# Optimization experiments

Hardware: AMD Instinct MI355X
Metric: run time of the kernel (lower is better)

Reference implementation:

```python
import jax, jax.numpy as jnp
import numpy as np

B, S, D, H = 2, 2048, 1024, 16
HD = D // H  # head depth


def setup_inputs() -> dict:
    key = jax.random.key(0)
    ks = jax.random.split(key, 8)
    scale = 0.02
    K = jax.random.normal(ks[0], (B, S, D), jnp.float32)
    V = jax.random.normal(ks[1], (B, S, D), jnp.float32)
    Q = jax.random.normal(ks[2], (B, S, D), jnp.float32)
    # causal additive mask: 1.0 where attention is disallowed (strict upper triangle)
    mask = jnp.broadcast_to(
        jnp.triu(jnp.ones((S, S), jnp.float32), k=1)[None, None, :, :], (B, 1, S, S)
    )
    Wk = jax.random.normal(ks[3], (D, D), jnp.float32) * scale
    Wv = jax.random.normal(ks[4], (D, D), jnp.float32) * scale
    Wq = jax.random.normal(ks[5], (D, D), jnp.float32) * scale
    Wo = jax.random.normal(ks[6], (D, D), jnp.float32) * scale
    z = jnp.zeros((D,), jnp.float32)
    return {"K": K, "V": V, "Q": Q, "mask": mask,
            "Wk": Wk, "bk": z, "Wv": Wv, "bv": z,
            "Wq": Wq, "bq": z, "Wo": Wo, "bo": z}


def _split_heads(x):  # [B,S,D] -> [B,H,S,HD]
    return x.reshape(B, S, H, HD).transpose(0, 2, 1, 3)


def reference(K, V, Q, mask, Wk, bk, Wv, bv, Wq, bq, Wo, bo):
    k = _split_heads(K @ Wk + bk)
    v = _split_heads(V @ Wv + bv)
    q = _split_heads(Q @ Wq + bq)
    # NOTE: source scales by sqrt(d_model), not sqrt(head_depth)
    logits = jnp.einsum("bhqd,bhkd->bhqk", q, k) / jnp.sqrt(jnp.float32(D))
    logits = logits + mask * (-1e9)
    attn = jax.nn.softmax(logits, axis=-1)
    out = jnp.einsum("bhqk,bhkd->bhqd", attn, v)  # [B,H,S,HD]
    out = out.transpose(0, 2, 1, 3).reshape(B, S, D)
    return out @ Wo + bo
```

## Files before the change

### kernel.cpp

```cpp
#include <hip/hip_runtime.h>
#include <hip/hip_bf16.h>

typedef unsigned short u16;
typedef unsigned int u32;
typedef unsigned long long u64;
typedef __attribute__((ext_vector_type(8))) __bf16 bf16x8;
typedef __attribute__((ext_vector_type(4))) float f32x4;

#define SEQ 2048
#define DM 1024
#define NH 16
#define HDim 64

__device__ __forceinline__ float bf_lo(u32 u) { return __uint_as_float(u << 16); }
__device__ __forceinline__ float bf_hi(u32 u) { return __uint_as_float(u & 0xffff0000u); }
__device__ __forceinline__ u16 f2bf(float f) {
    u32 u = __float_as_uint(f);
    u32 r = (u + 0x7fffu + ((u >> 16) & 1u)) >> 16;
    return (u16)r;
}
__device__ __forceinline__ float bf2f(u16 h) { return __uint_as_float(((u32)h) << 16); }

#define GLD16(g, l)                                                         \
    __builtin_amdgcn_global_load_lds(                                       \
        (const __attribute__((address_space(1))) void*)(g),                 \
        (__attribute__((address_space(3))) void*)(l), 16, 0, 0)

__device__ __forceinline__ bool detect_f32(const u32* q)
{
    const u32 w = q[threadIdx.x & 63];
    const int e0 = ((w & 0xffffu) >> 7) & 0xff;
    const int e1 = (w >> 23) & 0xff;
    const unsigned long long b = __ballot(e0 >= 0x90 || e1 >= 0x90);
    return b != 0ull;
}

__global__ __launch_bounds__(256)
void prep_all(const void* __restrict__ Qin, const void* __restrict__ Kin,
              const void* __restrict__ Vin,
              const void* __restrict__ w0, const void* __restrict__ w1,
              const void* __restrict__ w2, const void* __restrict__ w3,
              const void* __restrict__ b0, const void* __restrict__ b1,
              const void* __restrict__ b2, const void* __restrict__ b3,
              u16* __restrict__ Xall, u16* __restrict__ Wtall,
              u16* __restrict__ ball)
{
    __shared__ u16 T[64 * 66];
    const bool f = detect_f32((const u32*)Qin);
    const int t = threadIdx.x;
    const int bid = blockIdx.x;

    if (bid < 6144) {
        const int z = bid >> 11;
        const int bx = bid & 2047;
        const void* src = (z == 0) ? Qin : (z == 1) ? Kin : Vin;
        const size_t i0 = ((size_t)bx * 256 + t) * 8;
        u16* d = Xall + (size_t)z * 4194304 + i0;
        if (f) {
            const uint4* s = reinterpret_cast<const uint4*>((const float*)src + i0);
            uint4 a = s[0], b = s[1];
            u16 o[8];
            o[0] = f2bf(__uint_as_float(a.x)); o[1] = f2bf(__uint_as_float(a.y));
            o[2] = f2bf(__uint_as_float(a.z)); o[3] = f2bf(__uint_as_float(a.w));
            o[4] = f2bf(__uint_as_float(b.x)); o[5] = f2bf(__uint_as_float(b.y));
            o[6] = f2bf(__uint_as_float(b.z)); o[7] = f2bf(__uint_as_float(b.w));
            *reinterpret_cast<uint4*>(d) = *reinterpret_cast<const uint4*>(o);
        } else {
            *reinterpret_cast<uint4*>(d) =
                *reinterpret_cast<const uint4*>((const u16*)src + i0);
        }
    } else if (bid < 7168) {
        const int r = bid - 6144;
        const int z = r >> 8;
        const void* src = (z == 0) ? w0 : (z == 1) ? w1 : (z == 2) ? w2 : w3;
        const int n0 = ((r >> 4) & 15) * 64;
        const int k0 = (r & 15) * 64;
        const int c = t & 63, g = t >> 6;
        if (f) {
            const float* W = (const float*)src;
#pragma unroll
            for (int i = 0; i < 16; i++) {
                const int kl = g * 16 + i;
                T[kl * 66 + c] = f2bf(W[(size_t)(k0 + kl) * DM + n0 + c]);
            }
        } else {
            const u16* W = (const u16*)src;
#pragma unroll
            for (int i = 0; i < 16; i++) {
                const int kl = g * 16 + i;
                T[kl * 66 + c] = W[(size_t)(k0 + kl) * DM + n0 + c];
            }
        }
        __syncthreads();
        u16* dst = Wtall + (size_t)z * 1048576;
#pragma unroll
        for (int i = 0; i < 16; i++) {
            const int nl = g * 16 + i;
            dst[(size_t)(n0 + nl) * DM + k0 + c] = T[c * 66 + nl];
        }
    } else {
#pragma unroll
        for (int j = 0; j < 16; j++) {
            const int idx = t * 16 + j;
            const int z = idx >> 10, e = idx & 1023;
            const void* src = (z == 0) ? b0 : (z == 1) ? b1 : (z == 2) ? b2 : b3;
            ball[idx] = f ? f2bf(((const float*)src)[e]) : ((const u16*)src)[e];
        }
    }
}

__global__ __launch_bounds__(256)
void gemm128(const u16* __restrict__ Xall, const u16* __restrict__ Wtall,
             const u16* __restrict__ ball, u16* __restrict__ Yall,
             void* __restrict__ dout, int zbase, const u32* __restrict__ qdet)
{
    __shared__ __align__(16) u16 As[128 * 32];
    __shared__ __align__(16) u16 Bs[128 * 32];

    const int zz = zbase + blockIdx.z;
    const bool swp = (zz == 0) || (zz == 1);
    const u16* X  = Xall + ((zz == 3) ? 0 : (size_t)zz * 4194304);
    const u16* Wt = Wtall + (size_t)zz * 1048576;

    const int t    = threadIdx.x;
    const int w    = t >> 6;
    const int lane = t & 63;
    const int quad = lane >> 4;
    const int ln   = lane & 15;
    const int m0   = blockIdx.y * 128;
    const int n0   = blockIdx.x * 128;

    f32x4 acc[4][4];
#pragma unroll
    for (int i = 0; i < 4; i++)
#pragma unroll
        for (int j = 0; j < 4; j++) acc[i][j] = (f32x4){0.f, 0.f, 0.f, 0.f};

    const u16* ag = X  + (size_t)(m0 + w * 32 + (lane >> 2)) * DM + (lane & 3) * 8;
    const u16* bg = Wt + (size_t)(n0 + w * 32 + (lane >> 2)) * DM + (lane & 3) * 8;
    u16* al = &As[w * 1024];
    u16* bl = &Bs[w * 1024];

    const int wr = (w >> 1) * 64;
    const int wc = (w & 1) * 64;

    for (int kk = 0; kk < DM; kk += 32) {
        GLD16(ag,           al);
        GLD16(ag + 16 * DM, al + 512);
        GLD16(bg,           bl);
        GLD16(bg + 16 * DM, bl + 512);
        ag += 32; bg += 32;
        __syncthreads();

        bf16x8 af[4], bfr[4];
#pragma unroll
        for (int rt = 0; rt < 4; rt++)
            af[rt] = *reinterpret_cast<const bf16x8*>(&As[(wr + rt * 16 + ln) * 32 + quad * 8]);
#pragma unroll
        for (int ct = 0; ct < 4; ct++)
            bfr[ct] = *reinterpret_cast<const bf16x8*>(&Bs[(wc + ct * 16 + ln) * 32 + quad * 8]);
        if (swp) {
#pragma unroll
            for (int rt = 0; rt < 4; rt++)
#pragma unroll
                for (int ct = 0; ct < 4; ct++)
                    acc[rt][ct] = __builtin_amdgcn_mfma_f32_16x16x32_bf16(
                        bfr[ct], af[rt], acc[rt][ct], 0, 0, 0);
        } else {
#pragma unroll
            for (int rt = 0; rt < 4; rt++)
#pragma unroll
                for (int ct = 0; ct < 4; ct++)
                    acc[rt][ct] = __builtin_amdgcn_mfma_f32_16x16x32_bf16(
                        af[rt], bfr[ct], acc[rt][ct], 0, 0, 0);
        }
        __syncthreads();
    }

    u16* Y = Yall + (size_t)zz * 4194304;

    if (swp) {
        const float scale = (zz == 0) ? 0.03125f : 1.0f;
#pragma unroll
        for (int ct = 0; ct < 4; ct++) {
            const int nb = n0 + wc + ct * 16 + quad * 4;
            const int h = nb >> 6, hd = nb & (HDim - 1);
            float bv[4];
#pragma unroll
            for (int r = 0; r < 4; r++) bv[r] = bf2f(ball[zz * 1024 + nb + r]);
#pragma unroll
            for (int rt = 0; rt < 4; rt++) {
                const int m = m0 + wr + rt * 16 + ln;
                const int b = m >> 11, s = m & (SEQ - 1);
                u16 o4[4];
#pragma unroll
                for (int r = 0; r < 4; r++)
                    o4[r] = f2bf((acc[rt][ct][r] + bv[r]) * scale);
                *reinterpret_cast<u64*>(
                    Y + (((size_t)(b * NH + h)) * SEQ + s) * HDim + hd) =
                    *reinterpret_cast<const u64*>(o4);
            }
        }
    } else if (zz == 2) {
#pragma unroll
        for (int ct = 0; ct < 4; ct++) {
            const int n = n0 + wc + ct * 16 + ln;
            const float bv = bf2f(ball[zz * 1024 + n]);
            const int h = n >> 6, hd = n & (HDim - 1);
#pragma unroll
            for (int rt = 0; rt < 4; rt++) {
                const int m = m0 + wr + rt * 16 + quad * 4;
                const int b = m >> 11, s = m & (SEQ - 1);
                u16 o4[4];
#pragma unroll
                for (int r = 0; r < 4; r++) o4[r] = f2bf(acc[rt][ct][r] + bv);
                *reinterpret_cast<u64*>(
                    Y + (((size_t)(b * NH + h) * HDim + hd) * SEQ + s)) =
                    *reinterpret_cast<const u64*>(o4);
            }
        }
    } else {
        const bool f = detect_f32(qdet);
#pragma unroll
        for (int ct = 0; ct < 4; ct++) {
            const int n = n0 + wc + ct * 16 + ln;
            const float bv = bf2f(ball[zz * 1024 + n]);
#pragma unroll
            for (int rt = 0; rt < 4; rt++) {
                const int m = m0 + wr + rt * 16 + quad * 4;
#pragma unroll
                for (int r = 0; r < 4; r++) {
                    const float val = acc[rt][ct][r] + bv;
                    if (f) ((float*)dout)[(size_t)(m + r) * DM + n] = val;
                    else   ((u16*)dout)[(size_t)(m + r) * DM + n] = f2bf(val);
                }
            }
        }
    }
}

struct AttnAcc { f32x4 o[4]; float l[4]; };

__device__ __forceinline__ void attn_tile(
    const u16* __restrict__ Ks, const u16* __restrict__ Vs,
    u16* __restrict__ Ps, const bf16x8& qf0, const bf16x8& qf1,
    int kt, int rowb, int w, int quad, int ln, AttnAcc& a)
{
    f32x4 s[4];
#pragma unroll
    for (int ct = 0; ct < 4; ct++) {
        const u16* kr = &Ks[(ct * 16 + ln) * 72 + quad * 8];
        bf16x8 kf0 = *reinterpret_cast<const bf16x8*>(kr);
        bf16x8 kf1 = *reinterpret_cast<const bf16x8*>(kr + 32);
        f32x4 z = (f32x4){0.f, 0.f, 0.f, 0.f};
        z = __builtin_amdgcn_mfma_f32_16x16x32_bf16(qf0, kf0, z, 0, 0, 0);
        s[ct] = __builtin_amdgcn_mfma_f32_16x16x32_bf16(qf1, kf1, z, 0, 0, 0);
    }
#pragma unroll
    for (int ct = 0; ct < 4; ct++) {
        const int kcol = kt * 64 + ct * 16 + ln;
#pragma unroll
        for (int r = 0; r < 4; r++) {
            const float e = (kcol <= rowb + r) ? __expf(s[ct][r]) : 0.f;
            a.l[r] += e;
            Ps[(w * 16 + quad * 4 + r) * 68 + ct * 16 + ln] = f2bf(e);
        }
    }
#pragma unroll
    for (int ks = 0; ks < 2; ks++) {
        bf16x8 pf = *reinterpret_cast<const bf16x8*>(
            &Ps[(w * 16 + ln) * 68 + ks * 32 + quad * 8]);
#pragma unroll
        for (int nt = 0; nt < 4; nt++) {
            bf16x8 vf = *reinterpret_cast<const bf16x8*>(
                &Vs[(nt * 16 + ln) * 72 + ks * 32 + quad * 8]);
            a.o[nt] = __builtin_amdgcn_mfma_f32_16x16x32_bf16(pf, vf, a.o[nt], 0, 0, 0);
        }
    }
}

__global__ __launch_bounds__(256)
void attn_mfma(const u16* __restrict__ qh, const u16* __restrict__ kh,
               const u16* __restrict__ vt, u16* __restrict__ ctx)
{
    __shared__ __align__(16) u16 Ks[64 * 72];
    __shared__ __align__(16) u16 Vs[64 * 72];
    __shared__ __align__(16) u16 Ps[64 * 68];

    const int t    = threadIdx.x;
    const int i    = blockIdx.x;
    const int bh   = blockIdx.y;
    const int w    = t >> 6;
    const int lane = t & 63;
    const int quad = lane >> 4;
    const int ln   = lane & 15;
    const int qtH  = 31 - i;
    const int qtL  = i;

    const size_t kbase = (size_t)bh * SEQ * HDim;
    const size_t vbase = (size_t)bh * HDim * SEQ;

    const u16* qrH = qh + kbase + (size_t)(qtH * 64 + w * 16 + ln) * HDim;
    const bf16x8 qfH0 = *reinterpret_cast<const bf16x8*>(qrH + quad * 8);
    const bf16x8 qfH1 = *reinterpret_cast<const bf16x8*>(qrH + 32 + quad * 8);
    const u16* qrL = qh + kbase + (size_t)(qtL * 64 + w * 16 + ln) * HDim;
    const bf16x8 qfL0 = *reinterpret_cast<const bf16x8*>(qrL + quad * 8);
    const bf16x8 qfL1 = *reinterpret_cast<const bf16x8*>(qrL + 32 + quad * 8);

    AttnAcc aH, aL;
#pragma unroll
    for (int k = 0; k < 4; k++) {
        aH.o[k] = (f32x4){0.f, 0.f, 0.f, 0.f}; aH.l[k] = 0.f;
        aL.o[k] = (f32x4){0.f, 0.f, 0.f, 0.f}; aL.l[k] = 0.f;
    }

    const int srow = t >> 2;
    const int sc   = (t & 3) * 16;
    const int rowHb = qtH * 64 + w * 16 + quad * 4;
    const int rowLb = qtL * 64 + w * 16 + quad * 4;

    for (int kt = 0; kt <= qtH; kt++) {
        {
            const uint4* ks = reinterpret_cast<const uint4*>(
                kh + kbase + (size_t)(kt * 64 + srow) * HDim + sc);
            uint4* kd = reinterpret_cast<uint4*>(&Ks[srow * 72 + sc]);
            kd[0] = ks[0];
            kd[1] = ks[1];
            const uint4* vs = reinterpret_cast<const uint4*>(
                vt + vbase + (size_t)srow * SEQ + kt * 64 + sc);
            uint4* vd = reinterpret_cast<uint4*>(&Vs[srow * 72 + sc]);
            vd[0] = vs[0];
            vd[1] = vs[1];
        }
        __syncthreads();

        attn_tile(Ks, Vs, Ps, qfH0, qfH1, kt, rowHb, w, quad, ln, aH);
        if (kt <= qtL)
            attn_tile(Ks, Vs, Ps, qfL0, qfL1, kt, rowLb, w, quad, ln, aL);

        __syncthreads();
    }

#pragma unroll
    for (int m = 1; m < 16; m <<= 1) {
#pragma unroll
        for (int r = 0; r < 4; r++) {
            aH.l[r] += __shfl_xor(aH.l[r], m);
            aL.l[r] += __shfl_xor(aL.l[r], m);
        }
    }

    const int b = bh >> 4;
    const int h = bh & 15;
#pragma unroll
    for (int r = 0; r < 4; r++) {
        const float invH = 1.f / aH.l[r];
        const float invL = 1.f / aL.l[r];
        const int sH = qtH * 64 + w * 16 + quad * 4 + r;
        const int sL = qtL * 64 + w * 16 + quad * 4 + r;
        u16* dH = ctx + ((size_t)(b * SEQ + sH)) * DM + h * HDim + ln;
        u16* dL = ctx + ((size_t)(b * SEQ + sL)) * DM + h * HDim + ln;
#pragma unroll
        for (int nt = 0; nt < 4; nt++) {
            dH[nt * 16] = f2bf(aH.o[nt][r] * invH);
            dL[nt * 16] = f2bf(aL.o[nt][r] * invL);
        }
    }
}

__global__ __launch_bounds__(64)
void detect_dtype(const u32* __restrict__ q, int* __restrict__ flag)
{
    const int t = threadIdx.x;
    const u32 w = q[t];
    const int e0 = ((w & 0xffffu) >> 7) & 0xff;
    const int e1 = (w >> 23) & 0xff;
    const unsigned long long b = __ballot(e0 >= 0x90 || e1 >= 0x90);
    if (t == 0) *flag = (b != 0ull) ? 1 : 0;
}

__global__ __launch_bounds__(256)
void gemm_bias(const void* __restrict__ Xv, const void* __restrict__ Wv,
               const void* __restrict__ biasv, void* __restrict__ Yv,
               int M, int N, int K, int mode, int xsel, int wsel, int ysel,
               float scale, const int* __restrict__ flagp)
{
    __shared__ __align__(16) u16 As[64 * 32];
    __shared__ __align__(16) u16 Bs[64 * 40];

    const int f  = *flagp;
    const bool xf = (xsel != 0) && (f != 0);
    const bool wf = (wsel != 0) && (f != 0);
    const bool yf = (ysel != 0) && (f != 0);

    const u16*   Xb = (const u16*)Xv;
    const float* Xf = (const float*)Xv;
    const u16*   Wb = (const u16*)Wv;
    const float* Wf = (const float*)Wv;

    const int t    = threadIdx.x;
    const int m0   = blockIdx.y * 64;
    const int n0   = blockIdx.x * 64;
    const int w    = t >> 6;
    const int lane = t & 63;
    const int quad = lane >> 4;
    const int ln   = lane & 15;

    f32x4 acc[4];
#pragma unroll
    for (int i = 0; i < 4; i++) acc[i] = (f32x4){0.f, 0.f, 0.f, 0.f};

    const int a_row = t >> 2;
    const int a_c8  = (t & 3) * 8;
    const int b_n   = t & 63;
    const int b_k8  = (t >> 6) * 8;

    for (int kk = 0; kk < K; kk += 32) {
        const size_t aoff = (size_t)(m0 + a_row) * K + kk + a_c8;
        if (!xf) {
            *reinterpret_cast<uint4*>(&As[a_row * 32 + a_c8]) =
                *reinterpret_cast<const uint4*>(Xb + aoff);
        } else {
            const float* src = Xf + aoff;
            uint4 u0 = reinterpret_cast<const uint4*>(src)[0];
            uint4 u1 = reinterpret_cast<const uint4*>(src)[1];
            u16 tmp[8];
            tmp[0] = f2bf(__uint_as_float(u0.x));
            tmp[1] = f2bf(__uint_as_float(u0.y));
            tmp[2] = f2bf(__uint_as_float(u0.z));
            tmp[3] = f2bf(__uint_as_float(u0.w));
            tmp[4] = f2bf(__uint_as_float(u1.x));
            tmp[5] = f2bf(__uint_as_float(u1.y));
            tmp[6] = f2bf(__uint_as_float(u1.z));
            tmp[7] = f2bf(__uint_as_float(u1.w));
            *reinterpret_cast<uint4*>(&As[a_row * 32 + a_c8]) =
                *reinterpret_cast<const uint4*>(tmp);
        }
        u16 tmp[8];
        if (!wf) {
#pragma unroll
            for (int j = 0; j < 8; j++)
                tmp[j] = Wb[(size_t)(kk + b_k8 + j) * N + n0 + b_n];
        } else {
#pragma unroll
            for (int j = 0; j < 8; j++)
                tmp[j] = f2bf(Wf[(size_t)(kk + b_k8 + j) * N + n0 + b_n]);
        }
        *reinterpret_cast<uint4*>(&Bs[b_n * 40 + b_k8]) =
            *reinterpret_cast<const uint4*>(tmp);

        __syncthreads();

        bf16x8 bfrag = *reinterpret_cast<const bf16x8*>(&Bs[(w * 16 + ln) * 40 + quad * 8]);
#pragma unroll
        for (int rt = 0; rt < 4; rt++) {
            bf16x8 afrag = *reinterpret_cast<const bf16x8*>(&As[(rt * 16 + ln) * 32 + quad * 8]);
            acc[rt] = __builtin_amdgcn_mfma_f32_16x16x32_bf16(afrag, bfrag, acc[rt], 0, 0, 0);
        }
        __syncthreads();
    }

    const int n = n0 + w * 16 + ln;
    const float bv = wf ? ((const float*)biasv)[n] : bf2f(((const u16*)biasv)[n]);
#pragma unroll
    for (int rt = 0; rt < 4; rt++) {
        if (mode == 2) {
            const int m = m0 + rt * 16 + quad * 4;
            const int b = m >> 11;
            const int s = m & (SEQ - 1);
            const int h = n >> 6;
            const int hd = n & (HDim - 1);
            u16 o4[4];
#pragma unroll
            for (int r = 0; r < 4; r++) o4[r] = f2bf((acc[rt][r] + bv) * scale);
            *reinterpret_cast<u64*>(
                (u16*)Yv + (((size_t)(b * NH + h) * HDim + hd) * SEQ + s)) =
                *reinterpret_cast<const u64*>(o4);
        } else {
#pragma unroll
            for (int r = 0; r < 4; r++) {
                const int m = m0 + rt * 16 + quad * 4 + r;
                const float val = (acc[rt][r] + bv) * scale;
                if (mode == 0) {
                    if (yf) ((float*)Yv)[(size_t)m * N + n] = val;
                    else    ((u16*)Yv)[(size_t)m * N + n] = f2bf(val);
                } else {
                    const int b = m >> 11;
                    const int s = m & (SEQ - 1);
                    const int h = n >> 6;
                    const int hd = n & (HDim - 1);
                    ((u16*)Yv)[(((size_t)(b * NH + h)) * SEQ + s) * HDim + hd] = f2bf(val);
                }
            }
        }
    }
}

extern "C" void kernel_launch(void* const* d_in, const int* in_sizes, int n_in,
                              void* d_out, int out_size, void* d_ws, size_t ws_size,
                              hipStream_t stream)
{
    const void* Kin = d_in[0];
    const void* Vin = d_in[1];
    const void* Qin = d_in[2];
    const void* Wk = d_in[4];
    const void* bk = d_in[5];
    const void* Wv = d_in[6];
    const void* bv = d_in[7];
    const void* Wq = d_in[8];
    const void* bq = d_in[9];
    const void* Wo = d_in[10];
    const void* bo = d_in[11];

    char* ws = (char*)d_ws;
    const size_t NEED = ((size_t)29360128 + 4096) * 2 + 256;

    if (ws_size >= NEED) {
        u16* Xall  = (u16*)ws;
        u16* Yall  = (u16*)ws + 12582912;
        u16* Wtall = (u16*)ws + 25165824;
        u16* ball  = (u16*)ws + 29360128;
        u16* qhp   = Yall;
        u16* khp   = Yall + 4194304;
        u16* vtp   = Yall + 8388608;
        u16* ctx   = Xall;

        hipLaunchKernelGGL(prep_all, dim3(7169), dim3(256), 0, stream,
                           Qin, Kin, Vin, Wq, Wk, Wv, Wo, bq, bk, bv, bo,
                           Xall, Wtall, ball);

        hipLaunchKernelGGL(gemm128, dim3(8, 32, 3), dim3(256), 0, stream,
                           Xall, Wtall, ball, Yall, (void*)0, 0, (const u32*)Qin);

        hipLaunchKernelGGL(attn_mfma, dim3(16, 2 * NH), dim3(256), 0,
                           stream, qhp, khp, vtp, ctx);

        hipLaunchKernelGGL(gemm128, dim3(8, 32, 1), dim3(256), 0, stream,
                           Xall, Wtall, ball, Yall, d_out, 3, (const u32*)Qin);
    } else {
        const size_t SEG = (size_t)2 * SEQ * DM * sizeof(u16);
        u16* qh  = (u16*)(ws);
        u16* khd = (u16*)(ws + SEG);
        u16* vtd = (u16*)(ws + 2 * SEG);
        u16* ctx = (u16*)(ws + 3 * SEG);
        int* flag = (int*)(ws + 4 * SEG);

        hipLaunchKernelGGL(detect_dtype, dim3(1), dim3(64), 0, stream,
                           (const u32*)Qin, flag);

        const int M = 2 * SEQ;
        dim3 ggrid(DM / 64, M / 64);
        dim3 gblk(256);

        hipLaunchKernelGGL(gemm_bias, ggrid, gblk, 0, stream, Qin, Wq, bq, qh,  M, DM, DM, 1, 1, 1, 0, 0.03125f, flag);
        hipLaunchKernelGGL(gemm_bias, ggrid, gblk, 0, stream, Kin, Wk, bk, khd, M, DM, DM, 1, 1, 1, 0, 1.0f,     flag);
        hipLaunchKernelGGL(gemm_bias, ggrid, gblk, 0, stream, Vin, Wv, bv, vtd, M, DM, DM, 2, 1, 1, 0, 1.0f,     flag);

        hipLaunchKernelGGL(attn_mfma, dim3(16, 2 * NH), dim3(256), 0,
                           stream, qh, khd, vtd, ctx);

        hipLaunchKernelGGL(gemm_bias, ggrid, gblk, 0, stream, ctx, Wo, bo, d_out, M, DM, DM, 0, 0, 1, 1, 1.0f, flag);
    }
}
```

Baseline: 281.0 us.

## Fuse pipeline into cooperative persistent megakernel with split-K attention and output GEMM

Replaces the four separate launches with one cooperative persistent kernel that runs prep, QKV projection, attention, merge, output projection and reduction as phases separated by grid-wide syncs. Attention is split along the key dimension into two chunks whose unnormalized partial outputs and row sums are merged afterwards, balancing the causal workload. The output GEMM is split along K into two fp32 partial buffers that are summed with the bias. This targets launch gaps and tail imbalance, at the cost of grid-sync overhead, extra partial-result memory traffic and extra bf16 rounding of partial outputs, with a multi-kernel fallback path.

```diff
diff --git a/kernel.cpp b/kernel.cpp
--- a/kernel.cpp
+++ b/kernel.cpp
@@ -1,5 +1,8 @@
 #include <hip/hip_runtime.h>
 #include <hip/hip_bf16.h>
+#include <hip/hip_cooperative_groups.h>
+
+namespace cg = cooperative_groups;
 
 typedef unsigned short u16;
 typedef unsigned int u32;
@@ -35,21 +38,14 @@
     return b != 0ull;
 }
 
-__global__ __launch_bounds__(256)
-void prep_all(const void* __restrict__ Qin, const void* __restrict__ Kin,
-              const void* __restrict__ Vin,
-              const void* __restrict__ w0, const void* __restrict__ w1,
-              const void* __restrict__ w2, const void* __restrict__ w3,
-              const void* __restrict__ b0, const void* __restrict__ b1,
-              const void* __restrict__ b2, const void* __restrict__ b3,
-              u16* __restrict__ Xall, u16* __restrict__ Wtall,
-              u16* __restrict__ ball)
-{
-    __shared__ u16 T[64 * 66];
-    const bool f = detect_f32((const u32*)Qin);
-    const int t = threadIdx.x;
-    const int bid = blockIdx.x;
-
+
+__device__ __forceinline__ void prep_unit(
+    int bid, bool f, int t,
+    const void* Qin, const void* Kin, const void* Vin,
+    const void* w0, const void* w1, const void* w2, const void* w3,
+    const void* b0, const void* b1, const void* b2, const void* b3,
+    u16* Xall, u16* Wtall, u16* ball, u16* T)
+{
     if (bid < 6144) {
         const int z = bid >> 11;
         const int bx = bid & 2047;
@@ -107,28 +103,18 @@
             ball[idx] = f ? f2bf(((const float*)src)[e]) : ((const u16*)src)[e];
         }
     }
-}
-
-__global__ __launch_bounds__(256)
-void gemm128(const u16* __restrict__ Xall, const u16* __restrict__ Wtall,
-             const u16* __restrict__ ball, u16* __restrict__ Yall,
-             void* __restrict__ dout, int zbase, const u32* __restrict__ qdet)
-{
-    __shared__ __align__(16) u16 As[128 * 32];
-    __shared__ __align__(16) u16 Bs[128 * 32];
-
-    const int zz = zbase + blockIdx.z;
-    const bool swp = (zz == 0) || (zz == 1);
-    const u16* X  = Xall + ((zz == 3) ? 0 : (size_t)zz * 4194304);
-    const u16* Wt = Wtall + (size_t)zz * 1048576;
-
-    const int t    = threadIdx.x;
-    const int w    = t >> 6;
-    const int lane = t & 63;
-    const int quad = lane >> 4;
-    const int ln   = lane & 15;
-    const int m0   = blockIdx.y * 128;
-    const int n0   = blockIdx.x * 128;
+    __syncthreads();
+}
+
+__device__ __forceinline__ void proj_unit(
+    int zz, int m0, int n0, const u16* __restrict__ X,
+    const u16* __restrict__ Wt, const u16* __restrict__ bseg,
+    u16* __restrict__ Y, u16* SM, int t)
+{
+    u16* As = SM;
+    u16* Bs = SM + 4096;
+    const bool swp = (zz != 2);
+    const int w = t >> 6, lane = t & 63, quad = lane >> 4, ln = lane & 15;
 
     f32x4 acc[4][4];
 #pragma unroll
@@ -138,9 +124,8 @@
 
     const u16* ag = X  + (size_t)(m0 + w * 32 + (lane >> 2)) * DM + (lane & 3) * 8;
     const u16* bg = Wt + (size_t)(n0 + w * 32 + (lane >> 2)) * DM + (lane & 3) * 8;
-    u16* al = &As[w * 1024];
-    u16* bl = &Bs[w * 1024];
-
+    u16* al = As + w * 1024;
+    u16* bl = Bs + w * 1024;
     const int wr = (w >> 1) * 64;
     const int wc = (w & 1) * 64;
 
@@ -177,8 +162,6 @@
         __syncthreads();
     }
 
-    u16* Y = Yall + (size_t)zz * 4194304;
-
     if (swp) {
         const float scale = (zz == 0) ? 0.03125f : 1.0f;
 #pragma unroll
@@ -187,7 +170,7 @@
             const int h = nb >> 6, hd = nb & (HDim - 1);
             float bv[4];
 #pragma unroll
-            for (int r = 0; r < 4; r++) bv[r] = bf2f(ball[zz * 1024 + nb + r]);
+            for (int r = 0; r < 4; r++) bv[r] = bf2f(bseg[nb + r]);
 #pragma unroll
             for (int rt = 0; rt < 4; rt++) {
                 const int m = m0 + wr + rt * 16 + ln;
@@ -201,11 +184,11 @@
                     *reinterpret_cast<const u64*>(o4);
             }
         }
-    } else if (zz == 2) {
+    } else {
 #pragma unroll
         for (int ct = 0; ct < 4; ct++) {
             const int n = n0 + wc + ct * 16 + ln;
-            const float bv = bf2f(ball[zz * 1024 + n]);
+            const float bv = bf2f(bseg[n]);
             const int h = n >> 6, hd = n & (HDim - 1);
 #pragma unroll
             for (int rt = 0; rt < 4; rt++) {
@@ -219,32 +202,13 @@
                     *reinterpret_cast<const u64*>(o4);
             }
         }
-    } else {
-        const bool f = detect_f32(qdet);
-#pragma unroll
-        for (int ct = 0; ct < 4; ct++) {
-            const int n = n0 + wc + ct * 16 + ln;
-            const float bv = bf2f(ball[zz * 1024 + n]);
-#pragma unroll
-            for (int rt = 0; rt < 4; rt++) {
-                const int m = m0 + wr + rt * 16 + quad * 4;
-#pragma unroll
-                for (int r = 0; r < 4; r++) {
-                    const float val = acc[rt][ct][r] + bv;
-                    if (f) ((float*)dout)[(size_t)(m + r) * DM + n] = val;
-                    else   ((u16*)dout)[(size_t)(m + r) * DM + n] = f2bf(val);
-                }
-            }
-        }
-    }
-}
-
-struct AttnAcc { f32x4 o[4]; float l[4]; };
-
-__device__ __forceinline__ void attn_tile(
+    }
+}
+
+__device__ __forceinline__ void attn_tile2(
     const u16* __restrict__ Ks, const u16* __restrict__ Vs,
     u16* __restrict__ Ps, const bf16x8& qf0, const bf16x8& qf1,
-    int kt, int rowb, int w, int quad, int ln, AttnAcc& a)
+    int kt, int qrow, int w, int quad, int ln, f32x4* o, float& l)
 {
     f32x4 s[4];
 #pragma unroll
@@ -253,49 +217,54 @@
         bf16x8 kf0 = *reinterpret_cast<const bf16x8*>(kr);
         bf16x8 kf1 = *reinterpret_cast<const bf16x8*>(kr + 32);
         f32x4 z = (f32x4){0.f, 0.f, 0.f, 0.f};
-        z = __builtin_amdgcn_mfma_f32_16x16x32_bf16(qf0, kf0, z, 0, 0, 0);
-        s[ct] = __builtin_amdgcn_mfma_f32_16x16x32_bf16(qf1, kf1, z, 0, 0, 0);
+        z = __builtin_amdgcn_mfma_f32_16x16x32_bf16(kf0, qf0, z, 0, 0, 0);
+        s[ct] = __builtin_amdgcn_mfma_f32_16x16x32_bf16(kf1, qf1, z, 0, 0, 0);
     }
 #pragma unroll
     for (int ct = 0; ct < 4; ct++) {
-        const int kcol = kt * 64 + ct * 16 + ln;
+        u16 o4[4];
 #pragma unroll
         for (int r = 0; r < 4; r++) {
-            const float e = (kcol <= rowb + r) ? __expf(s[ct][r]) : 0.f;
-            a.l[r] += e;
-            Ps[(w * 16 + quad * 4 + r) * 68 + ct * 16 + ln] = f2bf(e);
-        }
+            const int kcol = kt * 64 + ct * 16 + quad * 4 + r;
+            const float e = (kcol <= qrow) ? __expf(s[ct][r]) : 0.f;
+            l += e;
+            o4[r] = f2bf(e);
+        }
+        *reinterpret_cast<u64*>(&Ps[(w * 16 + ln) * 72 + ct * 16 + quad * 4]) =
+            *reinterpret_cast<const u64*>(o4);
     }
 #pragma unroll
     for (int ks = 0; ks < 2; ks++) {
         bf16x8 pf = *reinterpret_cast<const bf16x8*>(
-            &Ps[(w * 16 + ln) * 68 + ks * 32 + quad * 8]);
+            &Ps[(w * 16 + ln) * 72 + ks * 32 + quad * 8]);
 #pragma unroll
         for (int nt = 0; nt < 4; nt++) {
             bf16x8 vf = *reinterpret_cast<const bf16x8*>(
                 &Vs[(nt * 16 + ln) * 72 + ks * 32 + quad * 8]);
-            a.o[nt] = __builtin_amdgcn_mfma_f32_16x16x32_bf16(pf, vf, a.o[nt], 0, 0, 0);
-        }
-    }
-}
-
-__global__ __launch_bounds__(256)
-void attn_mfma(const u16* __restrict__ qh, const u16* __restrict__ kh,
-               const u16* __restrict__ vt, u16* __restrict__ ctx)
-{
-    __shared__ __align__(16) u16 Ks[64 * 72];
-    __shared__ __align__(16) u16 Vs[64 * 72];
-    __shared__ __align__(16) u16 Ps[64 * 68];
-
-    const int t    = threadIdx.x;
-    const int i    = blockIdx.x;
-    const int bh   = blockIdx.y;
+            o[nt] = __builtin_amdgcn_mfma_f32_16x16x32_bf16(pf, vf, o[nt], 0, 0, 0);
+        }
+    }
+}
+
+__device__ __forceinline__ void attn_unit(
+    int i, int bh, int c,
+    const u16* __restrict__ qh, const u16* __restrict__ kh,
+    const u16* __restrict__ vt, u16* __restrict__ Opart,
+    float* __restrict__ Lpart, u16* SM, int t)
+{
+    u16* Ks = SM;
+    u16* Vs = SM + 4608;
+    u16* Ps = SM + 9216;
+
     const int w    = t >> 6;
     const int lane = t & 63;
     const int quad = lane >> 4;
     const int ln   = lane & 15;
     const int qtH  = 31 - i;
     const int qtL  = i;
+    const int m    = (i >= 8) ? 8 : 16 - i;
+    const int kt0  = c ? m : 0;
+    const int kt1  = c ? (qtH + 1) : m;
 
     const size_t kbase = (size_t)bh * SEQ * HDim;
     const size_t vbase = (size_t)bh * HDim * SEQ;
@@ -307,19 +276,20 @@
     const bf16x8 qfL0 = *reinterpret_cast<const bf16x8*>(qrL + quad * 8);
     const bf16x8 qfL1 = *reinterpret_cast<const bf16x8*>(qrL + 32 + quad * 8);
 
-    AttnAcc aH, aL;
+    f32x4 oH[4], oL[4];
+    float lH = 0.f, lL = 0.f;
 #pragma unroll
     for (int k = 0; k < 4; k++) {
-        aH.o[k] = (f32x4){0.f, 0.f, 0.f, 0.f}; aH.l[k] = 0.f;
-        aL.o[k] = (f32x4){0.f, 0.f, 0.f, 0.f}; aL.l[k] = 0.f;
+        oH[k] = (f32x4){0.f, 0.f, 0.f, 0.f};
+        oL[k] = (f32x4){0.f, 0.f, 0.f, 0.f};
     }
 
     const int srow = t >> 2;
     const int sc   = (t & 3) * 16;
-    const int rowHb = qtH * 64 + w * 16 + quad * 4;
-    const int rowLb = qtL * 64 + w * 16 + quad * 4;
-
-    for (int kt = 0; kt <= qtH; kt++) {
+    const int rowH = qtH * 64 + w * 16 + ln;
+    const int rowL = qtL * 64 + w * 16 + ln;
+
+    for (int kt = kt0; kt < kt1; kt++) {
         {
             const uint4* ks = reinterpret_cast<const uint4*>(
                 kh + kbase + (size_t)(kt * 64 + srow) * HDim + sc);
@@ -334,166 +304,263 @@
         }
         __syncthreads();
 
-        attn_tile(Ks, Vs, Ps, qfH0, qfH1, kt, rowHb, w, quad, ln, aH);
+        attn_tile2(Ks, Vs, Ps, qfH0, qfH1, kt, rowH, w, quad, ln, oH, lH);
         if (kt <= qtL)
-            attn_tile(Ks, Vs, Ps, qfL0, qfL1, kt, rowLb, w, quad, ln, aL);
+            attn_tile2(Ks, Vs, Ps, qfL0, qfL1, kt, rowL, w, quad, ln, oL, lL);
 
         __syncthreads();
     }
 
-#pragma unroll
-    for (int m = 1; m < 16; m <<= 1) {
-#pragma unroll
-        for (int r = 0; r < 4; r++) {
-            aH.l[r] += __shfl_xor(aH.l[r], m);
-            aL.l[r] += __shfl_xor(aL.l[r], m);
-        }
-    }
-
-    const int b = bh >> 4;
-    const int h = bh & 15;
+    lH += __shfl_xor(lH, 16); lH += __shfl_xor(lH, 32);
+    lL += __shfl_xor(lL, 16); lL += __shfl_xor(lL, 32);
+
+    const size_t cb = ((size_t)c * 32 + bh) * SEQ;
+    if (lane < 16) {
+        Lpart[cb + qtH * 64 + w * 16 + lane] = lH;
+        Lpart[cb + qtL * 64 + w * 16 + lane] = lL;
+    }
 #pragma unroll
     for (int r = 0; r < 4; r++) {
-        const float invH = 1.f / aH.l[r];
-        const float invL = 1.f / aL.l[r];
-        const int sH = qtH * 64 + w * 16 + quad * 4 + r;
-        const int sL = qtL * 64 + w * 16 + quad * 4 + r;
-        u16* dH = ctx + ((size_t)(b * SEQ + sH)) * DM + h * HDim + ln;
-        u16* dL = ctx + ((size_t)(b * SEQ + sL)) * DM + h * HDim + ln;
+        const int rH = qtH * 64 + w * 16 + quad * 4 + r;
+        const int rL = qtL * 64 + w * 16 + quad * 4 + r;
+        u16* dH = Opart + (cb + rH) * HDim + ln;
+        u16* dL = Opart + (cb + rL) * HDim + ln;
 #pragma unroll
         for (int nt = 0; nt < 4; nt++) {
-            dH[nt * 16] = f2bf(aH.o[nt][r] * invH);
-            dL[nt * 16] = f2bf(aL.o[nt][r] * invL);
-        }
-    }
-}
-
-__global__ __launch_bounds__(64)
-void detect_dtype(const u32* __restrict__ q, int* __restrict__ flag)
-{
+            dH[nt * 16] = f2bf(oH[nt][r]);
+            dL[nt * 16] = f2bf(oL[nt][r]);
+        }
+    }
+}
+
+__device__ __forceinline__ void merge_unit(
+    u32 tid8, const u16* __restrict__ Opart, const float* __restrict__ Lpart,
+    u16* __restrict__ ctx)
+{
+    const int d8 = (int)(tid8 & 7);
+    const int s  = (int)((tid8 >> 3) & (SEQ - 1));
+    const int bh = (int)(tid8 >> 14);
+    const size_t CSTR = (size_t)32 * SEQ * HDim;
+
+    const uint4 a = *reinterpret_cast<const uint4*>(Opart + (size_t)tid8 * 8);
+    const uint4 b = *reinterpret_cast<const uint4*>(Opart + CSTR + (size_t)tid8 * 8);
+    const float l0 = Lpart[(size_t)bh * SEQ + s];
+    const float l1 = Lpart[(size_t)32 * SEQ + (size_t)bh * SEQ + s];
+    const float inv = 1.f / (l0 + l1);
+
+    const u32 aw[4] = {a.x, a.y, a.z, a.w};
+    const u32 bw[4] = {b.x, b.y, b.z, b.w};
+    u32 ow[4];
+#pragma unroll
+    for (int p = 0; p < 4; p++) {
+        const float lo = (bf_lo(aw[p]) + bf_lo(bw[p])) * inv;
+        const float hi = (bf_hi(aw[p]) + bf_hi(bw[p])) * inv;
+        ow[p] = (u32)f2bf(lo) | ((u32)f2bf(hi) << 16);
+    }
+    const int bb = bh >> 4, h = bh & 15;
+    *reinterpret_cast<uint4*>(
+        ctx + ((size_t)(bb * SEQ + s)) * DM + h * HDim + d8 * 8) =
+        *reinterpret_cast<const uint4*>(ow);
+}
+
+__device__ __forceinline__ void outp_unit(
+    int kc, int mi, int ni, const u16* __restrict__ ctx,
+    const u16* __restrict__ Wt, float* __restrict__ P, u16* SM, int t)
+{
+    u16* As = SM;
+    u16* Bs = SM + 4096;
+    const int w = t >> 6, lane = t & 63, quad = lane >> 4, ln = lane & 15;
+    const int m0 = mi * 128, n0 = ni * 64, k0 = kc * 512;
+
+    f32x4 acc[4][2];
+#pragma unroll
+    for (int i = 0; i < 4; i++)
+#pragma unroll
+        for (int j = 0; j < 2; j++) acc[i][j] = (f32x4){0.f, 0.f, 0.f, 0.f};
+
+    const u16* ag = ctx + (size_t)(m0 + w * 32 + (lane >> 2)) * DM + k0 + (lane & 3) * 8;
+    const u16* bg = Wt + (size_t)(n0 + w * 16 + (lane >> 2)) * DM + k0 + (lane & 3) * 8;
+    u16* al = As + w * 1024;
+    u16* bl = Bs + w * 512;
+    const int wr = (w >> 1) * 64;
+    const int wc = (w & 1) * 32;
+
+    for (int kk = 0; kk < 512; kk += 32) {
+        GLD16(ag,           al);
+        GLD16(ag + 16 * DM, al + 512);
+        GLD16(bg,           bl);
+        ag += 32; bg += 32;
+        __syncthreads();
+
+        bf16x8 af[4], bfr[2];
+#pragma unroll
+        for (int rt = 0; rt < 4; rt++)
+            af[rt] = *reinterpret_cast<const bf16x8*>(&As[(wr + rt * 16 + ln) * 32 + quad * 8]);
+#pragma unroll
+        for (int ct = 0; ct < 2; ct++)
+            bfr[ct] = *reinterpret_cast<const bf16x8*>(&Bs[(wc + ct * 16 + ln) * 32 + quad * 8]);
+#pragma unroll
+        for (int rt = 0; rt < 4; rt++)
+#pragma unroll
+            for (int ct = 0; ct < 2; ct++)
+                acc[rt][ct] = __builtin_amdgcn_mfma_f32_16x16x32_bf16(
+                    bfr[ct], af[rt], acc[rt][ct], 0, 0, 0);
+        __syncthreads();
+    }
+
+#pragma unroll
+    for (int rt = 0; rt < 4; rt++) {
+        const int m = m0 + wr + rt * 16 + ln;
+#pragma unroll
+        for (int ct = 0; ct < 2; ct++) {
+            *reinterpret_cast<f32x4*>(
+                &P[(size_t)m * DM + n0 + wc + ct * 16 + quad * 4]) = acc[rt][ct];
+        }
+    }
+}
+
+__device__ __forceinline__ void reduce_unit(
+    u32 u, const float* __restrict__ P0, const float* __restrict__ P1,
+    const u16* __restrict__ bo, bool f, void* __restrict__ dout)
+{
+    const int n = (int)(u & 255) * 4;
+    const f32x4 a = *reinterpret_cast<const f32x4*>(P0 + (size_t)u * 4);
+    const f32x4 b = *reinterpret_cast<const f32x4*>(P1 + (size_t)u * 4);
+    f32x4 v;
+#pragma unroll
+    for (int j = 0; j < 4; j++) v[j] = a[j] + b[j] + bf2f(bo[n + j]);
+    if (f) {
+        *(reinterpret_cast<f32x4*>(dout) + u) = v;
+    } else {
+        u16 o4[4];
+#pragma unroll
+        for (int j = 0; j < 4; j++) o4[j] = f2bf(v[j]);
+        *reinterpret_cast<u64*>((u16*)dout + (size_t)u * 4) =
+            *reinterpret_cast<const u64*>(o4);
+    }
+}
+
+__global__ __launch_bounds__(256, 4)
+void mega(const void* Qin, const void* Kin, const void* Vin,
+          const void* w0, const void* w1, const void* w2, const void* w3,
+          const void* b0, const void* b1, const void* b2, const void* b3,
+          u16* Xall, u16* Wtall, u16* ball, void* dout)
+{
+    __shared__ __align__(16) u16 SM[13824];
+    cg::grid_group grid = cg::this_grid();
+    const bool f = detect_f32((const u32*)Qin);
     const int t = threadIdx.x;
-    const u32 w = q[t];
-    const int e0 = ((w & 0xffffu) >> 7) & 0xff;
-    const int e1 = (w >> 23) & 0xff;
-    const unsigned long long b = __ballot(e0 >= 0x90 || e1 >= 0x90);
-    if (t == 0) *flag = (b != 0ull) ? 1 : 0;
+    const u32 g = gridDim.x;
+
+    for (u32 u = blockIdx.x; u < 7169; u += g)
+        prep_unit((int)u, f, t, Qin, Kin, Vin, w0, w1, w2, w3,
+                  b0, b1, b2, b3, Xall, Wtall, ball, SM);
+    __threadfence();
+    grid.sync();
+
+    u16* Yall = Xall + 12582912;
+    for (u32 u = blockIdx.x; u < 768; u += g) {
+        const int z = (int)(u >> 8);
+        const int r = (int)(u & 255);
+        proj_unit(z, (r & 31) * 128, (r >> 5) * 128,
+                  Xall + (size_t)z * 4194304, Wtall + (size_t)z * 1048576,
+                  ball + z * 1024, Yall + (size_t)z * 4194304, SM, t);
+    }
+    __threadfence();
+    grid.sync();
+
+    u16* Opart = Xall + 4194304;
+    float* Lpart = (float*)Wtall;
+    const u16* qh = Yall;
+    const u16* kh = Yall + 4194304;
+    const u16* vt = Yall + 8388608;
+    for (u32 u = blockIdx.x; u < 1024; u += g) {
+        const int c = (int)(u >> 9);
+        const int r = (int)(u & 511);
+        attn_unit(r & 15, r >> 4, c, qh, kh, vt, Opart, Lpart, SM, t);
+    }
+    __threadfence();
+    grid.sync();
+
+    u16* ctx = Xall;
+    for (u32 u = (u32)blockIdx.x * 256 + t; u < 524288; u += g * 256)
+        merge_unit(u, Opart, Lpart, ctx);
+    __threadfence();
+    grid.sync();
+
+    float* Pk0 = (float*)(Xall + 4194304);
+    float* Pk1 = (float*)(Xall + 12582912);
+    const u16* Wto = Wtall + (size_t)3 * 1048576;
+    for (u32 u = blockIdx.x; u < 1024; u += g) {
+        const int kc = (int)(u >> 9);
+        const int r = (int)(u & 511);
+        outp_unit(kc, r & 31, r >> 5, ctx, Wto, kc ? Pk1 : Pk0, SM, t);
+    }
+    __threadfence();
+    grid.sync();
+
+    const u16* bo = ball + 3072;
+    for (u32 u = (u32)blockIdx.x * 256 + t; u < 1048576; u += g * 256)
+        reduce_unit(u, Pk0, Pk1, bo, f, dout);
 }
 
 __global__ __launch_bounds__(256)
-void gemm_bias(const void* __restrict__ Xv, const void* __restrict__ Wv,
-               const void* __restrict__ biasv, void* __restrict__ Yv,
-               int M, int N, int K, int mode, int xsel, int wsel, int ysel,
-               float scale, const int* __restrict__ flagp)
-{
-    __shared__ __align__(16) u16 As[64 * 32];
-    __shared__ __align__(16) u16 Bs[64 * 40];
-
-    const int f  = *flagp;
-    const bool xf = (xsel != 0) && (f != 0);
-    const bool wf = (wsel != 0) && (f != 0);
-    const bool yf = (ysel != 0) && (f != 0);
-
-    const u16*   Xb = (const u16*)Xv;
-    const float* Xf = (const float*)Xv;
-    const u16*   Wb = (const u16*)Wv;
-    const float* Wf = (const float*)Wv;
-
-    const int t    = threadIdx.x;
-    const int m0   = blockIdx.y * 64;
-    const int n0   = blockIdx.x * 64;
-    const int w    = t >> 6;
-    const int lane = t & 63;
-    const int quad = lane >> 4;
-    const int ln   = lane & 15;
-
-    f32x4 acc[4];
-#pragma unroll
-    for (int i = 0; i < 4; i++) acc[i] = (f32x4){0.f, 0.f, 0.f, 0.f};
-
-    const int a_row = t >> 2;
-    const int a_c8  = (t & 3) * 8;
-    const int b_n   = t & 63;
-    const int b_k8  = (t >> 6) * 8;
-
-    for (int kk = 0; kk < K; kk += 32) {
-        const size_t aoff = (size_t)(m0 + a_row) * K + kk + a_c8;
-        if (!xf) {
-            *reinterpret_cast<uint4*>(&As[a_row * 32 + a_c8]) =
-                *reinterpret_cast<const uint4*>(Xb + aoff);
-        } else {
-            const float* src = Xf + aoff;
-            uint4 u0 = reinterpret_cast<const uint4*>(src)[0];
-            uint4 u1 = reinterpret_cast<const uint4*>(src)[1];
-            u16 tmp[8];
-            tmp[0] = f2bf(__uint_as_float(u0.x));
-            tmp[1] = f2bf(__uint_as_float(u0.y));
-            tmp[2] = f2bf(__uint_as_float(u0.z));
-            tmp[3] = f2bf(__uint_as_float(u0.w));
-            tmp[4] = f2bf(__uint_as_float(u1.x));
-            tmp[5] = f2bf(__uint_as_float(u1.y));
-            tmp[6] = f2bf(__uint_as_float(u1.z));
-            tmp[7] = f2bf(__uint_as_float(u1.w));
-            *reinterpret_cast<uint4*>(&As[a_row * 32 + a_c8]) =
-                *reinterpret_cast<const uint4*>(tmp);
-        }
-        u16 tmp[8];
-        if (!wf) {
-#pragma unroll
-            for (int j = 0; j < 8; j++)
-                tmp[j] = Wb[(size_t)(kk + b_k8 + j) * N + n0 + b_n];
-        } else {
-#pragma unroll
-            for (int j = 0; j < 8; j++)
-                tmp[j] = f2bf(Wf[(size_t)(kk + b_k8 + j) * N + n0 + b_n]);
-        }
-        *reinterpret_cast<uint4*>(&Bs[b_n * 40 + b_k8]) =
-            *reinterpret_cast<const uint4*>(tmp);
-
-        __syncthreads();
-
-        bf16x8 bfrag = *reinterpret_cast<const bf16x8*>(&Bs[(w * 16 + ln) * 40 + quad * 8]);
-#pragma unroll
-        for (int rt = 0; rt < 4; rt++) {
-            bf16x8 afrag = *reinterpret_cast<const bf16x8*>(&As[(rt * 16 + ln) * 32 + quad * 8]);
-            acc[rt] = __builtin_amdgcn_mfma_f32_16x16x32_bf16(afrag, bfrag, acc[rt], 0, 0, 0);
-        }
-        __syncthreads();
-    }
-
-    const int n = n0 + w * 16 + ln;
-    const float bv = wf ? ((const float*)biasv)[n] : bf2f(((const u16*)biasv)[n]);
-#pragma unroll
-    for (int rt = 0; rt < 4; rt++) {
-        if (mode == 2) {
-            const int m = m0 + rt * 16 + quad * 4;
-            const int b = m >> 11;
-            const int s = m & (SEQ - 1);
-            const int h = n >> 6;
-            const int hd = n & (HDim - 1);
-            u16 o4[4];
-#pragma unroll
-            for (int r = 0; r < 4; r++) o4[r] = f2bf((acc[rt][r] + bv) * scale);
-            *reinterpret_cast<u64*>(
-                (u16*)Yv + (((size_t)(b * NH + h) * HDim + hd) * SEQ + s)) =
-                *reinterpret_cast<const u64*>(o4);
-        } else {
-#pragma unroll
-            for (int r = 0; r < 4; r++) {
-                const int m = m0 + rt * 16 + quad * 4 + r;
-                const float val = (acc[rt][r] + bv) * scale;
-                if (mode == 0) {
-                    if (yf) ((float*)Yv)[(size_t)m * N + n] = val;
-                    else    ((u16*)Yv)[(size_t)m * N + n] = f2bf(val);
-                } else {
-                    const int b = m >> 11;
-                    const int s = m & (SEQ - 1);
-                    const int h = n >> 6;
-                    const int hd = n & (HDim - 1);
-                    ((u16*)Yv)[(((size_t)(b * NH + h)) * SEQ + s) * HDim + hd] = f2bf(val);
-                }
-            }
-        }
-    }
+void prep_k(const void* Qin, const void* Kin, const void* Vin,
+            const void* w0, const void* w1, const void* w2, const void* w3,
+            const void* b0, const void* b1, const void* b2, const void* b3,
+            u16* Xall, u16* Wtall, u16* ball)
+{
+    __shared__ __align__(16) u16 SM[4224];
+    const bool f = detect_f32((const u32*)Qin);
+    prep_unit(blockIdx.x, f, threadIdx.x, Qin, Kin, Vin, w0, w1, w2, w3,
+              b0, b1, b2, b3, Xall, Wtall, ball, SM);
+}
+
+__global__ __launch_bounds__(256)
+void proj_k(const u16* Xall, const u16* Wtall, const u16* ball, u16* Yall)
+{
+    __shared__ __align__(16) u16 SM[8192];
+    const u32 u = blockIdx.x;
+    const int z = (int)(u >> 8);
+    const int r = (int)(u & 255);
+    proj_unit(z, (r & 31) * 128, (r >> 5) * 128,
+              Xall + (size_t)z * 4194304, Wtall + (size_t)z * 1048576,
+              ball + z * 1024, Yall + (size_t)z * 4194304, SM, threadIdx.x);
+}
+
+__global__ __launch_bounds__(256)
+void attn_k(const u16* qh, const u16* kh, const u16* vt,
+            u16* Opart, float* Lpart)
+{
+    __shared__ __align__(16) u16 SM[13824];
+    const u32 u = blockIdx.x;
+    const int c = (int)(u >> 9);
+    const int r = (int)(u & 511);
+    attn_unit(r & 15, r >> 4, c, qh, kh, vt, Opart, Lpart, SM, threadIdx.x);
+}
+
+__global__ __launch_bounds__(256)
+void merge_k(const u16* Opart, const float* Lpart, u16* ctx)
+{
+    merge_unit((u32)blockIdx.x * 256 + threadIdx.x, Opart, Lpart, ctx);
+}
+
+__global__ __launch_bounds__(256)
+void outp_k(const u16* ctx, const u16* Wto, float* Pk0, float* Pk1)
+{
+    __shared__ __align__(16) u16 SM[6144];
+    const u32 u = blockIdx.x;
+    const int kc = (int)(u >> 9);
+    const int r = (int)(u & 511);
+    outp_unit(kc, r & 31, r >> 5, ctx, Wto, kc ? Pk1 : Pk0, SM, threadIdx.x);
+}
+
+__global__ __launch_bounds__(256)
+void reduce_k(const float* P0, const float* P1, const u16* bo,
+              const u32* qdet, void* dout)
+{
+    const bool f = detect_f32(qdet);
+    reduce_unit((u32)blockIdx.x * 256 + threadIdx.x, P0, P1, bo, f, dout);
 }
 
 extern "C" void kernel_launch(void* const* d_in, const int* in_sizes, int n_in,
@@ -512,53 +579,47 @@
     const void* Wo = d_in[10];
     const void* bo = d_in[11];
 
-    char* ws = (char*)d_ws;
-    const size_t NEED = ((size_t)29360128 + 4096) * 2 + 256;
-
-    if (ws_size >= NEED) {
-        u16* Xall  = (u16*)ws;
-        u16* Yall  = (u16*)ws + 12582912;
-        u16* Wtall = (u16*)ws + 25165824;
-        u16* ball  = (u16*)ws + 29360128;
-        u16* qhp   = Yall;
-        u16* khp   = Yall + 4194304;
-        u16* vtp   = Yall + 8388608;
-        u16* ctx   = Xall;
-
-        hipLaunchKernelGGL(prep_all, dim3(7169), dim3(256), 0, stream,
+    u16* Xall  = (u16*)d_ws;
+    u16* Wtall = Xall + 25165824;
+    u16* ball  = Xall + 29360128;
+    u16* Yall  = Xall + 12582912;
+    u16* ctx   = Xall;
+    u16* Opart = Xall + 4194304;
+    float* Lpart = (float*)Wtall;
+    float* Pk0 = (float*)(Xall + 4194304);
+    float* Pk1 = (float*)(Xall + 12582912);
+    u16* Wto = Wtall + (size_t)3 * 1048576;
+
+    int occ = 0;
+    hipError_t oe = hipOccupancyMaxActiveBlocksPerMultiprocessor(&occ, mega, 256, 0);
+    u32 gsize = (oe == hipSuccess && occ > 0) ? (u32)occ * 256u : 0u;
+    if (gsize > 1024u) gsize = 1024u;
+
+    bool done = false;
+    if (gsize >= 256u) {
+        void* args[] = {
+            (void*)&Qin, (void*)&Kin, (void*)&Vin,
+            (void*)&Wq, (void*)&Wk, (void*)&Wv, (void*)&Wo,
+            (void*)&bq, (void*)&bk, (void*)&bv, (void*)&bo,
+            (void*)&Xall, (void*)&Wtall, (void*)&ball, (void*)&d_out};
+        hipError_t le = hipLaunchCooperativeKernel(
+            mega, dim3(gsize), dim3(256), args, 0, stream);
+        done = (le == hipSuccess);
+    }
+
+    if (!done) {
+        hipLaunchKernelGGL(prep_k, dim3(7169), dim3(256), 0, stream,
                            Qin, Kin, Vin, Wq, Wk, Wv, Wo, bq, bk, bv, bo,
                            Xall, Wtall, ball);
-
-        hipLaunchKernelGGL(gemm128, dim3(8, 32, 3), dim3(256), 0, stream,
-                           Xall, Wtall, ball, Yall, (void*)0, 0, (const u32*)Qin);
-
-        hipLaunchKernelGGL(attn_mfma, dim3(16, 2 * NH), dim3(256), 0,
-                           stream, qhp, khp, vtp, ctx);
-
-        hipLaunchKernelGGL(gemm128, dim3(8, 32, 1), dim3(256), 0, stream,
-                           Xall, Wtall, ball, Yall, d_out, 3, (const u32*)Qin);
-    } else {
-        const size_t SEG = (size_t)2 * SEQ * DM * sizeof(u16);
-        u16* qh  = (u16*)(ws);
-        u16* khd = (u16*)(ws + SEG);
-        u16* vtd = (u16*)(ws + 2 * SEG);
-        u16* ctx = (u16*)(ws + 3 * SEG);
-        int* flag = (int*)(ws + 4 * SEG);
-
-        hipLaunchKernelGGL(detect_dtype, dim3(1), dim3(64), 0, stream,
-                           (const u32*)Qin, flag);
-
-        const int M = 2 * SEQ;
-        dim3 ggrid(DM / 64, M / 64);
-        dim3 gblk(256);
-
-        hipLaunchKernelGGL(gemm_bias, ggrid, gblk, 0, stream, Qin, Wq, bq, qh,  M, DM, DM, 1, 1, 1, 0, 0.03125f, flag);
-        hipLaunchKernelGGL(gemm_bias, ggrid, gblk, 0, stream, Kin, Wk, bk, khd, M, DM, DM, 1, 1, 1, 0, 1.0f,     flag);
-        hipLaunchKernelGGL(gemm_bias, ggrid, gblk, 0, stream, Vin, Wv, bv, vtd, M, DM, DM, 2, 1, 1, 0, 1.0f,     flag);
-
-        hipLaunchKernelGGL(attn_mfma, dim3(16, 2 * NH), dim3(256), 0,
-                           stream, qh, khd, vtd, ctx);
-
-        hipLaunchKernelGGL(gemm_bias, ggrid, gblk, 0, stream, ctx, Wo, bo, d_out, M, DM, DM, 0, 0, 1, 1, 1.0f, flag);
-    }
-}
+        hipLaunchKernelGGL(proj_k, dim3(768), dim3(256), 0, stream,
+                           Xall, Wtall, ball, Yall);
+        hipLaunchKernelGGL(attn_k, dim3(1024), dim3(256), 0, stream,
+                           Yall, Yall + 4194304, Yall + 8388608, Opart, Lpart);
+        hipLaunchKernelGGL(merge_k, dim3(2048), dim3(256), 0, stream,
+                           Opart, Lpart, ctx);
+        hipLaunchKernelGGL(outp_k, dim3(1024), dim3(256), 0, stream,
+                           ctx, Wto, Pk0, Pk1);
+        hipLaunchKernelGGL(reduce_k, dim3(4096), dim3(256), 0, stream,
+                           Pk0, Pk1, ball + 3072, (const u32*)Qin, d_out);
+    }
+}
```

Measured after the change: 1.057 ms. 3.76x slower.
